# Optimization experiments

Hardware: AMD Instinct MI355X
Metric: run time of the kernel (lower is better)

The kernel has to match this reference:

```python
import jax, jax.numpy as jnp
import numpy as np
from jax import lax

B, M, N = 16, 256, 8192
NUM_CLASSES = 80
IGNORED_CLASS_IDX = 80          # never occurs in [0,80); keeps the ignore branch faithful but inert
BATCH_SIZE_PER_IMAGE = 512
POSITIVE_FRACTION = 0.25
IOU_THRESHOLD = 0.5
NUM_FG = int(BATCH_SIZE_PER_IMAGE * POSITIVE_FRACTION)   # 128
NUM_BG = BATCH_SIZE_PER_IMAGE - NUM_FG                   # 384
NEG = jnp.float32(-1e30)


def _make_boxes(key, shape, img_size=1024.0, min_sz=16.0, max_sz=256.0):
    kc, ks = jax.random.split(key)
    ctr = jax.random.uniform(kc, shape + (2,), minval=0.0, maxval=img_size)
    wh = jax.random.uniform(ks, shape + (2,), minval=min_sz, maxval=max_sz)
    return jnp.concatenate([ctr - 0.5 * wh, ctr + 0.5 * wh], axis=-1)  # xyxy


def setup_inputs() -> dict:
    key = jax.random.key(0)
    k1, k2, k3, k4 = jax.random.split(key, 4)
    return {
        "gt_boxes": _make_boxes(k1, (B, M)),
        "gt_classes": jax.random.randint(k2, (B, M), 0, NUM_CLASSES).astype(jnp.int32),
        "proposal_boxes": _make_boxes(k3, (B, N)),
        "rand_priority": jax.random.uniform(k4, (B, N), dtype=jnp.float32),
    }


def pairwise_iou(gt, pr):
    # gt: [B,M,4], pr: [B,N,4] (x1,y1,x2,y2) -> iou [B,M,N]
    area_g = (gt[..., 2] - gt[..., 0]) * (gt[..., 3] - gt[..., 1])   # [B,M]
    area_p = (pr[..., 2] - pr[..., 0]) * (pr[..., 3] - pr[..., 1])   # [B,N]
    lt = jnp.maximum(gt[:, :, None, :2], pr[:, None, :, :2])         # [B,M,N,2]
    rb = jnp.minimum(gt[:, :, None, 2:], pr[:, None, :, 2:])
    wh = jnp.clip(rb - lt, 0.0)
    inter = wh[..., 0] * wh[..., 1]                                  # [B,M,N]
    union = area_g[:, :, None] + area_p[:, None, :] - inter
    return jnp.where(union > 0, inter / union, 0.0)


def _sample(mask, priority, k):
    # pick up to k True entries of mask, randomized by priority; returns (idx [B,k], valid [B,k])
    pri = jnp.where(mask, priority, NEG)
    top, idx = lax.top_k(pri, k)
    return idx, top > NEG


def reference(gt_boxes, gt_classes, proposal_boxes, rand_priority):
    iou = pairwise_iou(gt_boxes, proposal_boxes)          # [B,M,N]
    matched_vals = iou.max(axis=1)                        # [B,N]
    matched_idxs = iou.argmax(axis=1).astype(jnp.int32)   # [B,N]
    matched_labels = matched_vals >= IOU_THRESHOLD        # Matcher([0.5],[0,1])

    # _sample_proposals label assignment
    cls = jnp.take_along_axis(gt_classes, matched_idxs, axis=1)     # [B,N]
    cls = jnp.where(cls == IGNORED_CLASS_IDX, -1, cls)
    cls = jnp.where(~matched_labels, NUM_CLASSES, cls)              # background

    fg_mask = (cls >= 0) & (cls != NUM_CLASSES)
    bg_mask = cls == NUM_CLASSES
    fg_idx, fg_valid = _sample(fg_mask, rand_priority, NUM_FG)
    bg_idx, bg_valid = _sample(bg_mask, rand_priority, NUM_BG)

    sampled_idxs = jnp.concatenate([fg_idx, bg_idx], axis=1)        # [B,512]
    valid = jnp.concatenate([fg_valid, bg_valid], axis=1)
    sampled_classes = jnp.where(valid,
                                jnp.take_along_axis(cls, sampled_idxs, axis=1), -1)
    sampled_gt = jnp.where(valid,
                           jnp.take_along_axis(matched_idxs, sampled_idxs, axis=1), -1)
    return matched_vals, matched_idxs, sampled_idxs, sampled_classes, sampled_gt
```

## Files before the change

kernel.cpp:

```cpp
#include <hip/hip_runtime.h>
#include <stdint.h>

#define BATCH 16
#define MGT 256
#define NPROP 8192
#define NUM_CLASSES 80
#define IGNORED_CLASS 80
#define NUM_FG 128
#define NUM_BG 384
#define SENT 0xFFFFFFFFu

typedef unsigned long long u64;


__global__ __launch_bounds__(256) void match_kernel(
    const float* __restrict__ gt_boxes,
    const int*   __restrict__ gt_classes,
    const float* __restrict__ prop_boxes,
    float*       __restrict__ out,
    int*         __restrict__ cls_ws,
    int*         __restrict__ midx_ws)
{
#pragma clang fp contract(off)
    __shared__ float4 sbox[MGT];
    __shared__ float  sga[MGT];
    __shared__ u64    skey[128];

    const int b   = blockIdx.y;
    const int tid = threadIdx.x;

    {
        const float4 g = ((const float4*)gt_boxes)[(size_t)b * MGT + tid];
        sbox[tid] = g;
        sga[tid]  = (g.z - g.x) * (g.w - g.y);
    }
    __syncthreads();

    const int pl   = tid & 127;
    const int half = tid >> 7;
    const int n    = blockIdx.x * 128 + pl;
    const float4 p = ((const float4*)prop_boxes)[(size_t)b * NPROP + n];
    const float ap = (p.z - p.x) * (p.w - p.y);

    float best = -1.0f;
    int   bidx = 0;
    const int m0 = half * 128;
#pragma unroll 4
    for (int mm = 0; mm < 128; ++mm) {
        const int m = m0 + mm;
        const float4 g = sbox[m];
        const float ag = sga[m];
        float ltx = fmaxf(g.x, p.x);
        float lty = fmaxf(g.y, p.y);
        float rbx = fminf(g.z, p.z);
        float rby = fminf(g.w, p.w);
        float w = fmaxf(rbx - ltx, 0.0f);
        float h = fmaxf(rby - lty, 0.0f);
        float inter = w * h;
        float uni = (ag + ap) - inter;
        float iou = (uni > 0.0f) ? (inter / uni) : 0.0f;
        if (iou > best) { best = iou; bidx = m; }
    }
    u64 key = ((u64)__float_as_uint(best) << 32) | (uint32_t)(255 - bidx);
    if (half) skey[pl] = key;
    __syncthreads();
    if (half == 0) {
        u64 o = skey[pl];
        if (o > key) key = o;
        float bestf = __uint_as_float((uint32_t)(key >> 32));
        int   bi    = 255 - (int)(key & 0xFFu);

        const bool matched = (bestf >= 0.5f);
        int c = gt_classes[b * MGT + bi];
        if (c == IGNORED_CLASS) c = -1;
        if (!matched) c = NUM_CLASSES;

        const size_t on = (size_t)b * NPROP + n;
        out[on]                         = bestf;
        out[(size_t)BATCH * NPROP + on] = (float)bi;
        cls_ws[on]  = c;
        midx_ws[on] = bi;
    }
}

__device__ __forceinline__ uint32_t wave_incl_scan_u32(uint32_t x) {
#pragma unroll
    for (int d = 1; d < 64; d <<= 1) {
        uint32_t y = __shfl_up(x, d, 64);
        if ((threadIdx.x & 63) >= d) x += y;
    }
    return x;
}

__device__ __forceinline__ uint32_t block_excl_scan(uint32_t s, uint32_t* wsums) {
    const int tid = threadIdx.x, lane = tid & 63, wid = tid >> 6;
    __syncthreads();
    uint32_t incl = wave_incl_scan_u32(s);
    if (lane == 63) wsums[wid] = incl;
    __syncthreads();
    if (wid == 0) {
        uint32_t w  = (lane < 16) ? wsums[lane] : 0u;
        uint32_t wi = wave_incl_scan_u32(w);
        if (lane < 16) wsums[lane] = wi - w;
    }
    __syncthreads();
    return wsums[wid] + (incl - s);
}

__device__ __forceinline__ void scan_and_find(uint32_t* hist, uint32_t* wsums,
                                              uint32_t kk, uint32_t* sc_b, uint32_t* sc_p) {
    const int tid  = threadIdx.x;
    __syncthreads();
    const int base = tid * 4;
    uint32_t v0 = hist[base], v1 = hist[base+1], v2 = hist[base+2], v3 = hist[base+3];
    uint32_t pre = block_excl_scan(v0+v1+v2+v3, wsums);
    uint32_t i0 = pre+v0, i1 = i0+v1, i2 = i1+v2, i3 = i2+v3;
    hist[base] = i0; hist[base+1] = i1; hist[base+2] = i2; hist[base+3] = i3;
    __syncthreads();
    uint32_t prev = (base == 0) ? 0u : hist[base-1];
    uint32_t inc[4] = {i0, i1, i2, i3};
#pragma unroll
    for (int j = 0; j < 4; ++j) {
        if (inc[j] >= kk && prev < kk) { *sc_b = (uint32_t)(base+j); *sc_p = prev; }
        prev = inc[j];
    }
    __syncthreads();
}

__global__ __launch_bounds__(1024) void sample_kernel(
    const float* __restrict__ pri_f,
    const int*   __restrict__ cls_ws,
    const int*   __restrict__ midx_ws,
    float*       __restrict__ out)
{
    __shared__ uint32_t h32[NPROP];
    __shared__ uint32_t hist[4096];
    __shared__ uint32_t wsums[16];
    __shared__ uint32_t sc[8];
    __shared__ u64      sel[NUM_BG];

    const int tid  = threadIdx.x;
    const int b    = blockIdx.x >> 1;
    const int pass = blockIdx.x & 1;
    const int K    = pass ? NUM_BG : NUM_FG;
    const int off  = pass ? NUM_FG : 0;

    const float* pri  = pri_f   + (size_t)b * NPROP;
    const int*   cls  = cls_ws  + (size_t)b * NPROP;
    const int*   midx = midx_ws + (size_t)b * NPROP;

    float* s_idx = out + (size_t)2 * BATCH * NPROP + (size_t)b * 512;
    float* s_cls = s_idx + (size_t)BATCH * 512;
    float* s_gt  = s_idx + (size_t)2 * BATCH * 512;

    if (tid < 8) sc[tid] = 0u;
    for (int i = tid; i < 4096; i += 1024) hist[i] = 0u;
    __syncthreads();

    uint32_t creal = 0;
#pragma unroll
    for (int it = 0; it < 8; ++it) {
        const int i = tid + it * 1024;
        const int c = cls[i];
        const bool m = pass ? (c == NUM_CLASSES) : (c >= 0 && c != NUM_CLASSES);
        uint32_t v = SENT;
        if (m) {
            uint32_t bits = __float_as_uint(pri[i]);
            uint32_t ord  = (bits & 0x80000000u) ? ~bits : (bits | 0x80000000u);
            v = ~ord;
        }
        h32[i] = v;
        u64 bal = __ballot(m);
        if ((tid & 63) == 0) creal += __popcll(bal);
    }
    if ((tid & 63) == 0 && creal) atomicAdd(&sc[6], creal);
    __syncthreads();
    const uint32_t C    = sc[6];
    const uint32_t ksel = (C < (uint32_t)K) ? C : (uint32_t)K;

    if (C > 0) {
        for (int i = tid; i < NPROP; i += 1024) {
            uint32_t v = h32[i];
            if (v < 0x80000000u) atomicAdd(&hist[v >> 20], 1u);
        }
        scan_and_find(hist, wsums, ksel, &sc[0], &sc[1]);
        const uint32_t b1 = sc[0], p1 = sc[1];
        const uint32_t k2 = ksel - p1;
        for (int i = tid; i < 4096; i += 1024) hist[i] = 0u;
        __syncthreads();

        for (int i = tid; i < NPROP; i += 1024) {
            uint32_t v = h32[i];
            if ((v >> 20) == b1) atomicAdd(&hist[(v >> 8) & 0xFFFu], 1u);
        }
        scan_and_find(hist, wsums, k2, &sc[2], &sc[3]);
        const uint32_t b2 = sc[2], p2 = sc[3];
        const uint32_t k3 = k2 - p2;
        for (int i = tid; i < 4096; i += 1024) hist[i] = 0u;
        __syncthreads();

        const uint32_t top24 = (b1 << 12) | b2;
        for (int i = tid; i < NPROP; i += 1024) {
            uint32_t v = h32[i];
            if ((v >> 8) == top24) atomicAdd(&hist[v & 0xFFu], 1u);
        }
        scan_and_find(hist, wsums, k3, &sc[4], &sc[5]);
        const uint32_t b3 = sc[4], p3 = sc[5];
        const uint32_t k4 = k3 - p3;
        const uint32_t Hstar = (b1 << 20) | (b2 << 8) | b3;

        uint32_t hv[8]; uint32_t ssum = 0;
        const int cbase = tid * 8;
#pragma unroll
        for (int j = 0; j < 8; ++j) { hv[j] = h32[cbase + j]; ssum += (hv[j] == Hstar); }
        uint32_t run = block_excl_scan(ssum, wsums);
#pragma unroll
        for (int j = 0; j < 8; ++j) {
            bool take = false;
            if (hv[j] < Hstar) take = true;
            else if (hv[j] == Hstar) { take = (run < k4); ++run; }
            if (take) {
                uint32_t pos = atomicAdd(&sc[7], 1u);
                sel[pos] = ((u64)hv[j] << 32) | (uint32_t)(cbase + j);
            }
        }
        __syncthreads();
        const uint32_t S = sc[7];

        for (uint32_t j = tid; j < S; j += 1024) {
            const u64 kj = sel[j];
            uint32_t r = 0;
            for (uint32_t i = 0; i < S; ++i) r += (sel[i] < kj);
            const uint32_t idx = (uint32_t)kj;
            s_idx[off + r] = (float)idx;
            s_cls[off + r] = (float)cls[idx];
            s_gt[off + r]  = (float)midx[idx];
        }
    }

    if (ksel < (uint32_t)K) {
        const uint32_t F = (uint32_t)K - ksel;
        uint32_t hv[8]; uint32_t ssum = 0;
        const int cbase = tid * 8;
#pragma unroll
        for (int j = 0; j < 8; ++j) { hv[j] = h32[cbase + j]; ssum += (hv[j] == SENT); }
        uint32_t run = block_excl_scan(ssum, wsums);
#pragma unroll
        for (int j = 0; j < 8; ++j) {
            if (hv[j] == SENT) {
                if (run < F) {
                    const int slot = off + (int)ksel + (int)run;
                    s_idx[slot] = (float)(cbase + j);
                    s_cls[slot] = -1.0f;
                    s_gt[slot]  = -1.0f;
                }
                ++run;
            }
        }
    }
}

extern "C" void kernel_launch(void* const* d_in, const int* in_sizes, int n_in,
                              void* d_out, int out_size, void* d_ws, size_t ws_size,
                              hipStream_t stream) {
    const float* gt_boxes   = (const float*)d_in[0];
    const int*   gt_classes = (const int*)d_in[1];
    const float* prop_boxes = (const float*)d_in[2];
    const float* rand_pri   = (const float*)d_in[3];
    float* out = (float*)d_out;

    int* cls_ws  = (int*)d_ws;
    int* midx_ws = cls_ws + (size_t)BATCH * NPROP;

    dim3 grid1(NPROP / 128, BATCH);
    match_kernel<<<grid1, 256, 0, stream>>>(gt_boxes, gt_classes, prop_boxes,
                                            out, cls_ws, midx_ws);

    sample_kernel<<<BATCH * 2, 1024, 0, stream>>>(rand_pri, cls_ws, midx_ws, out);
}
```

Before: 105.9 us.

## Fuse matching and sampling into one kernel with last-block-done sampling

Merges the IoU match kernel and the top-k sampling kernel into a single launch. The last block to finish each image, detected with an atomic counter, runs both the fg and bg sampling passes with 256 threads. Also packs class and match index into one int, reads gt boxes from global instead of LDS, and adds an early-out threshold test that skips the divide when a candidate cannot beat the current best. Risks: sampling now runs serially with fewer threads per image, and the divide-skip heuristic could in principle change argmax ties.

Result: slower. 194.7 us (+83.9%).

```diff
diff --git a/kernel.cpp b/kernel.cpp
--- a/kernel.cpp
+++ b/kernel.cpp
@@ -9,79 +9,24 @@
 #define NUM_FG 128
 #define NUM_BG 384
 #define SENT 0xFFFFFFFFu
+#define BS 256
+#define CHUNKS_PER_ROW (NPROP / BS)
+#define NUM_BLOCKS (BATCH * CHUNKS_PER_ROW)
 
 typedef unsigned long long u64;
 
 
-__global__ __launch_bounds__(256) void match_kernel(
-    const float* __restrict__ gt_boxes,
-    const int*   __restrict__ gt_classes,
-    const float* __restrict__ prop_boxes,
-    float*       __restrict__ out,
-    int*         __restrict__ cls_ws,
-    int*         __restrict__ midx_ws)
-{
-#pragma clang fp contract(off)
-    __shared__ float4 sbox[MGT];
-    __shared__ float  sga[MGT];
-    __shared__ u64    skey[128];
-
-    const int b   = blockIdx.y;
-    const int tid = threadIdx.x;
-
-    {
-        const float4 g = ((const float4*)gt_boxes)[(size_t)b * MGT + tid];
-        sbox[tid] = g;
-        sga[tid]  = (g.z - g.x) * (g.w - g.y);
-    }
-    __syncthreads();
-
-    const int pl   = tid & 127;
-    const int half = tid >> 7;
-    const int n    = blockIdx.x * 128 + pl;
-    const float4 p = ((const float4*)prop_boxes)[(size_t)b * NPROP + n];
-    const float ap = (p.z - p.x) * (p.w - p.y);
-
-    float best = -1.0f;
-    int   bidx = 0;
-    const int m0 = half * 128;
-#pragma unroll 4
-    for (int mm = 0; mm < 128; ++mm) {
-        const int m = m0 + mm;
-        const float4 g = sbox[m];
-        const float ag = sga[m];
-        float ltx = fmaxf(g.x, p.x);
-        float lty = fmaxf(g.y, p.y);
-        float rbx = fminf(g.z, p.z);
-        float rby = fminf(g.w, p.w);
-        float w = fmaxf(rbx - ltx, 0.0f);
-        float h = fmaxf(rby - lty, 0.0f);
-        float inter = w * h;
-        float uni = (ag + ap) - inter;
-        float iou = (uni > 0.0f) ? (inter / uni) : 0.0f;
-        if (iou > best) { best = iou; bidx = m; }
-    }
-    u64 key = ((u64)__float_as_uint(best) << 32) | (uint32_t)(255 - bidx);
-    if (half) skey[pl] = key;
-    __syncthreads();
-    if (half == 0) {
-        u64 o = skey[pl];
-        if (o > key) key = o;
-        float bestf = __uint_as_float((uint32_t)(key >> 32));
-        int   bi    = 255 - (int)(key & 0xFFu);
-
-        const bool matched = (bestf >= 0.5f);
-        int c = gt_classes[b * MGT + bi];
-        if (c == IGNORED_CLASS) c = -1;
-        if (!matched) c = NUM_CLASSES;
-
-        const size_t on = (size_t)b * NPROP + n;
-        out[on]                         = bestf;
-        out[(size_t)BATCH * NPROP + on] = (float)bi;
-        cls_ws[on]  = c;
-        midx_ws[on] = bi;
-    }
-}
+struct SampleSmem {
+    uint32_t h32[NPROP];
+    uint32_t hist[4096];
+    uint32_t wsums[4];
+    uint32_t sc[8];
+    u64      sel[NUM_BG];
+};
+union Smem {
+    SampleSmem s;
+    struct { float sga[MGT]; } m;
+};
 
 __device__ __forceinline__ uint32_t wave_incl_scan_u32(uint32_t x) {
 #pragma unroll
@@ -92,76 +37,64 @@
     return x;
 }
 
-__device__ __forceinline__ uint32_t block_excl_scan(uint32_t s, uint32_t* wsums) {
+__device__ uint32_t block_excl_scan(uint32_t s, uint32_t* wsums) {
     const int tid = threadIdx.x, lane = tid & 63, wid = tid >> 6;
     __syncthreads();
     uint32_t incl = wave_incl_scan_u32(s);
     if (lane == 63) wsums[wid] = incl;
     __syncthreads();
     if (wid == 0) {
-        uint32_t w  = (lane < 16) ? wsums[lane] : 0u;
+        uint32_t w  = (lane < 4) ? wsums[lane] : 0u;
         uint32_t wi = wave_incl_scan_u32(w);
-        if (lane < 16) wsums[lane] = wi - w;
+        if (lane < 4) wsums[lane] = wi - w;
     }
     __syncthreads();
     return wsums[wid] + (incl - s);
 }
 
-__device__ __forceinline__ void scan_and_find(uint32_t* hist, uint32_t* wsums,
-                                              uint32_t kk, uint32_t* sc_b, uint32_t* sc_p) {
-    const int tid  = threadIdx.x;
-    __syncthreads();
-    const int base = tid * 4;
-    uint32_t v0 = hist[base], v1 = hist[base+1], v2 = hist[base+2], v3 = hist[base+3];
-    uint32_t pre = block_excl_scan(v0+v1+v2+v3, wsums);
-    uint32_t i0 = pre+v0, i1 = i0+v1, i2 = i1+v2, i3 = i2+v3;
-    hist[base] = i0; hist[base+1] = i1; hist[base+2] = i2; hist[base+3] = i3;
-    __syncthreads();
-    uint32_t prev = (base == 0) ? 0u : hist[base-1];
-    uint32_t inc[4] = {i0, i1, i2, i3};
-#pragma unroll
-    for (int j = 0; j < 4; ++j) {
-        if (inc[j] >= kk && prev < kk) { *sc_b = (uint32_t)(base+j); *sc_p = prev; }
-        prev = inc[j];
-    }
-    __syncthreads();
-}
-
-__global__ __launch_bounds__(1024) void sample_kernel(
-    const float* __restrict__ pri_f,
-    const int*   __restrict__ cls_ws,
-    const int*   __restrict__ midx_ws,
-    float*       __restrict__ out)
+__device__ void scan_and_find(uint32_t* hist, uint32_t* wsums, uint32_t kk,
+                              uint32_t* sc_b, uint32_t* sc_p) {
+    const int tid = threadIdx.x;
+    __syncthreads();
+    const int base = tid * 16;
+    uint32_t v[16]; uint32_t tot = 0;
+#pragma unroll
+    for (int j = 0; j < 16; ++j) { v[j] = hist[base + j]; tot += v[j]; }
+    uint32_t prev = block_excl_scan(tot, wsums);
+#pragma unroll
+    for (int j = 0; j < 16; ++j) {
+        uint32_t inc = prev + v[j];
+        if (inc >= kk && prev < kk) { *sc_b = (uint32_t)(base + j); *sc_p = prev; }
+        prev = inc;
+    }
+    __syncthreads();
+}
+
+__device__ void sample_pass(SampleSmem* S, int b, int pass,
+                            const float* __restrict__ pri_f,
+                            const int* __restrict__ packed,
+                            float* __restrict__ out)
 {
-    __shared__ uint32_t h32[NPROP];
-    __shared__ uint32_t hist[4096];
-    __shared__ uint32_t wsums[16];
-    __shared__ uint32_t sc[8];
-    __shared__ u64      sel[NUM_BG];
-
-    const int tid  = threadIdx.x;
-    const int b    = blockIdx.x >> 1;
-    const int pass = blockIdx.x & 1;
-    const int K    = pass ? NUM_BG : NUM_FG;
-    const int off  = pass ? NUM_FG : 0;
-
-    const float* pri  = pri_f   + (size_t)b * NPROP;
-    const int*   cls  = cls_ws  + (size_t)b * NPROP;
-    const int*   midx = midx_ws + (size_t)b * NPROP;
+    const int tid = threadIdx.x;
+    const int K   = pass ? NUM_BG : NUM_FG;
+    const int off = pass ? NUM_FG : 0;
+
+    const float* pri = pri_f  + (size_t)b * NPROP;
+    const int*   pk  = packed + (size_t)b * NPROP;
 
     float* s_idx = out + (size_t)2 * BATCH * NPROP + (size_t)b * 512;
     float* s_cls = s_idx + (size_t)BATCH * 512;
     float* s_gt  = s_idx + (size_t)2 * BATCH * 512;
 
-    if (tid < 8) sc[tid] = 0u;
-    for (int i = tid; i < 4096; i += 1024) hist[i] = 0u;
+    if (tid < 8) S->sc[tid] = 0u;
+    for (int i = tid; i < 4096; i += BS) S->hist[i] = 0u;
     __syncthreads();
 
     uint32_t creal = 0;
 #pragma unroll
-    for (int it = 0; it < 8; ++it) {
-        const int i = tid + it * 1024;
-        const int c = cls[i];
+    for (int it = 0; it < NPROP / BS; ++it) {
+        const int i = tid + it * BS;
+        const int c = (pk[i] & 0xFFFF) - 1;
         const bool m = pass ? (c == NUM_CLASSES) : (c >= 0 && c != NUM_CLASSES);
         uint32_t v = SENT;
         if (m) {
@@ -169,85 +102,86 @@
             uint32_t ord  = (bits & 0x80000000u) ? ~bits : (bits | 0x80000000u);
             v = ~ord;
         }
-        h32[i] = v;
+        S->h32[i] = v;
         u64 bal = __ballot(m);
         if ((tid & 63) == 0) creal += __popcll(bal);
     }
-    if ((tid & 63) == 0 && creal) atomicAdd(&sc[6], creal);
-    __syncthreads();
-    const uint32_t C    = sc[6];
+    if ((tid & 63) == 0 && creal) atomicAdd(&S->sc[6], creal);
+    __syncthreads();
+    const uint32_t C    = S->sc[6];
     const uint32_t ksel = (C < (uint32_t)K) ? C : (uint32_t)K;
 
     if (C > 0) {
-        for (int i = tid; i < NPROP; i += 1024) {
-            uint32_t v = h32[i];
-            if (v < 0x80000000u) atomicAdd(&hist[v >> 20], 1u);
-        }
-        scan_and_find(hist, wsums, ksel, &sc[0], &sc[1]);
-        const uint32_t b1 = sc[0], p1 = sc[1];
+        for (int i = tid; i < NPROP; i += BS) {
+            uint32_t v = S->h32[i];
+            if (v < 0x80000000u) atomicAdd(&S->hist[v >> 20], 1u);
+        }
+        scan_and_find(S->hist, S->wsums, ksel, &S->sc[0], &S->sc[1]);
+        const uint32_t b1 = S->sc[0], p1 = S->sc[1];
         const uint32_t k2 = ksel - p1;
-        for (int i = tid; i < 4096; i += 1024) hist[i] = 0u;
+        for (int i = tid; i < 4096; i += BS) S->hist[i] = 0u;
         __syncthreads();
 
-        for (int i = tid; i < NPROP; i += 1024) {
-            uint32_t v = h32[i];
-            if ((v >> 20) == b1) atomicAdd(&hist[(v >> 8) & 0xFFFu], 1u);
-        }
-        scan_and_find(hist, wsums, k2, &sc[2], &sc[3]);
-        const uint32_t b2 = sc[2], p2 = sc[3];
+        for (int i = tid; i < NPROP; i += BS) {
+            uint32_t v = S->h32[i];
+            if ((v >> 20) == b1) atomicAdd(&S->hist[(v >> 8) & 0xFFFu], 1u);
+        }
+        scan_and_find(S->hist, S->wsums, k2, &S->sc[2], &S->sc[3]);
+        const uint32_t b2 = S->sc[2], p2 = S->sc[3];
         const uint32_t k3 = k2 - p2;
-        for (int i = tid; i < 4096; i += 1024) hist[i] = 0u;
+        for (int i = tid; i < 4096; i += BS) S->hist[i] = 0u;
         __syncthreads();
 
         const uint32_t top24 = (b1 << 12) | b2;
-        for (int i = tid; i < NPROP; i += 1024) {
-            uint32_t v = h32[i];
-            if ((v >> 8) == top24) atomicAdd(&hist[v & 0xFFu], 1u);
-        }
-        scan_and_find(hist, wsums, k3, &sc[4], &sc[5]);
-        const uint32_t b3 = sc[4], p3 = sc[5];
+        for (int i = tid; i < NPROP; i += BS) {
+            uint32_t v = S->h32[i];
+            if ((v >> 8) == top24) atomicAdd(&S->hist[v & 0xFFu], 1u);
+        }
+        scan_and_find(S->hist, S->wsums, k3, &S->sc[4], &S->sc[5]);
+        const uint32_t b3 = S->sc[4], p3 = S->sc[5];
         const uint32_t k4 = k3 - p3;
         const uint32_t Hstar = (b1 << 20) | (b2 << 8) | b3;
 
-        uint32_t hv[8]; uint32_t ssum = 0;
-        const int cbase = tid * 8;
-#pragma unroll
-        for (int j = 0; j < 8; ++j) { hv[j] = h32[cbase + j]; ssum += (hv[j] == Hstar); }
-        uint32_t run = block_excl_scan(ssum, wsums);
-#pragma unroll
-        for (int j = 0; j < 8; ++j) {
+        uint32_t hv[32]; uint32_t ssum = 0;
+        const int cbase = tid * 32;
+#pragma unroll
+        for (int j = 0; j < 32; ++j) { hv[j] = S->h32[cbase + j]; ssum += (hv[j] == Hstar); }
+        uint32_t run = block_excl_scan(ssum, S->wsums);
+#pragma unroll
+        for (int j = 0; j < 32; ++j) {
             bool take = false;
             if (hv[j] < Hstar) take = true;
             else if (hv[j] == Hstar) { take = (run < k4); ++run; }
             if (take) {
-                uint32_t pos = atomicAdd(&sc[7], 1u);
-                sel[pos] = ((u64)hv[j] << 32) | (uint32_t)(cbase + j);
+                uint32_t pos = atomicAdd(&S->sc[7], 1u);
+                S->sel[pos] = ((u64)hv[j] << 32) | (uint32_t)(cbase + j);
             }
         }
         __syncthreads();
-        const uint32_t S = sc[7];
-
-        for (uint32_t j = tid; j < S; j += 1024) {
-            const u64 kj = sel[j];
+        const uint32_t Scnt = S->sc[7];
+
+        for (uint32_t j = tid; j < Scnt; j += BS) {
+            const u64 kj = S->sel[j];
             uint32_t r = 0;
-            for (uint32_t i = 0; i < S; ++i) r += (sel[i] < kj);
+            for (uint32_t i = 0; i < Scnt; ++i) r += (S->sel[i] < kj);
             const uint32_t idx = (uint32_t)kj;
+            const int pv = pk[idx];
             s_idx[off + r] = (float)idx;
-            s_cls[off + r] = (float)cls[idx];
-            s_gt[off + r]  = (float)midx[idx];
+            s_cls[off + r] = (float)((pv & 0xFFFF) - 1);
+            s_gt[off + r]  = (float)(pv >> 16);
         }
     }
 
     if (ksel < (uint32_t)K) {
         const uint32_t F = (uint32_t)K - ksel;
-        uint32_t hv[8]; uint32_t ssum = 0;
-        const int cbase = tid * 8;
-#pragma unroll
-        for (int j = 0; j < 8; ++j) { hv[j] = h32[cbase + j]; ssum += (hv[j] == SENT); }
-        uint32_t run = block_excl_scan(ssum, wsums);
-#pragma unroll
-        for (int j = 0; j < 8; ++j) {
-            if (hv[j] == SENT) {
+        uint32_t hv2[32]; uint32_t sv = 0;
+        const int cbase = tid * 32;
+#pragma unroll
+        for (int j = 0; j < 32; ++j) { hv2[j] = S->h32[cbase + j]; sv += (hv2[j] == SENT); }
+        uint32_t run = block_excl_scan(sv, S->wsums);
+#pragma unroll
+        for (int j = 0; j < 32; ++j) {
+            if (hv2[j] == SENT) {
                 if (run < F) {
                     const int slot = off + (int)ksel + (int)run;
                     s_idx[slot] = (float)(cbase + j);
@@ -258,6 +192,78 @@
             }
         }
     }
+    __syncthreads();
+}
+
+__global__ __launch_bounds__(64) void init_kernel(int* __restrict__ done) {
+    if (threadIdx.x < BATCH) done[threadIdx.x] = 0;
+}
+
+__global__ __launch_bounds__(BS) void fused_kernel(
+    const float* __restrict__ gt_boxes, const int* __restrict__ gt_classes,
+    const float* __restrict__ prop_boxes, const float* __restrict__ pri,
+    float* __restrict__ out, int* __restrict__ packed, int* __restrict__ done)
+{
+#pragma clang fp contract(off)
+    __shared__ Smem sm;
+    __shared__ int s_old;
+
+    const int tid = threadIdx.x;
+    const int t   = blockIdx.x;
+    const int b   = t >> 5;
+    const int n   = ((t & 31) << 8) | tid;
+
+    const float4* gt4 = (const float4*)gt_boxes + (size_t)b * MGT;
+    {
+        float4 g = gt4[tid];
+        sm.m.sga[tid] = (g.z - g.x) * (g.w - g.y);
+    }
+    __syncthreads();
+
+    const float4 p = ((const float4*)prop_boxes)[(size_t)b * NPROP + n];
+    const float ap = (p.z - p.x) * (p.w - p.y);
+
+    float best = 0.0f;
+    int   bidx = 0;
+    for (int m = 0; m < MGT; ++m) {
+        const float4 g = gt4[m];
+        float ltx = fmaxf(g.x, p.x);
+        float lty = fmaxf(g.y, p.y);
+        float rbx = fminf(g.z, p.z);
+        float rby = fminf(g.w, p.w);
+        float w = fmaxf(rbx - ltx, 0.0f);
+        float h = fmaxf(rby - lty, 0.0f);
+        float inter = w * h;
+        float s   = sm.m.sga[m] + ap;
+        float uni = s - inter;
+        float thr = (best * uni) * 0.9999996f;
+        if (inter > thr) {
+            float iou = (uni > 0.0f) ? (inter / uni) : 0.0f;
+            if (iou > best) { best = iou; bidx = m; }
+        }
+    }
+
+    const bool matched = (best >= 0.5f);
+    int c = gt_classes[b * MGT + bidx];
+    if (c == IGNORED_CLASS) c = -1;
+    if (!matched) c = NUM_CLASSES;
+
+    const size_t on = (size_t)b * NPROP + n;
+    out[on]                         = best;
+    out[(size_t)BATCH * NPROP + on] = (float)bidx;
+    packed[on] = (bidx << 16) | (c + 1);
+
+    __syncthreads();
+    if (tid == 0) {
+        __threadfence();
+        s_old = atomicAdd(&done[b], 1);
+    }
+    __syncthreads();
+    if (s_old != CHUNKS_PER_ROW - 1) return;
+
+    __threadfence();
+    sample_pass(&sm.s, b, 0, pri, packed, out);
+    sample_pass(&sm.s, b, 1, pri, packed, out);
 }
 
 extern "C" void kernel_launch(void* const* d_in, const int* in_sizes, int n_in,
@@ -269,12 +275,10 @@
     const float* rand_pri   = (const float*)d_in[3];
     float* out = (float*)d_out;
 
-    int* cls_ws  = (int*)d_ws;
-    int* midx_ws = cls_ws + (size_t)BATCH * NPROP;
-
-    dim3 grid1(NPROP / 128, BATCH);
-    match_kernel<<<grid1, 256, 0, stream>>>(gt_boxes, gt_classes, prop_boxes,
-                                            out, cls_ws, midx_ws);
-
-    sample_kernel<<<BATCH * 2, 1024, 0, stream>>>(rand_pri, cls_ws, midx_ws, out);
-}
+    int* packed = (int*)d_ws;
+    int* done   = packed + (size_t)BATCH * NPROP;
+
+    init_kernel<<<1, 64, 0, stream>>>(done);
+    fused_kernel<<<NUM_BLOCKS, BS, 0, stream>>>(
+        gt_boxes, gt_classes, prop_boxes, rand_pri, out, packed, done);
+}
```
